# Optimization experiments

Hardware: AMD Instinct MI355X
Metric: run time of the kernel (lower is better)

The kernel has to match this reference:

```python
import jax, jax.numpy as jnp
import numpy as np

NUM_HEADS = 8
ATTN_DIM = 64

def setup_inputs() -> dict:
    key = jax.random.key(0)
    ks = jax.random.split(key, 16)
    C = ATTN_DIM
    inp = {
        "rgb_fea": jax.random.normal(ks[0], (2, C, 48, 48), jnp.float32),
        "depth_fea": jax.random.normal(ks[1], (2, 1, 24, 24), jnp.float32),
        # expend_conv: Conv2d(1 -> C, k=1), with bias (torch default)
        "w_exp": jax.random.normal(ks[2], (C, 1), jnp.float32) * 0.2,
        "b_exp": jax.random.normal(ks[3], (C,), jnp.float32) * 0.02,
        # q/k/v linears (no bias), weights stored torch-style [out, in]
        "w_rgb_q": jax.random.normal(ks[4], (C, C), jnp.float32) * (C ** -0.5),
        "w_rgb_k": jax.random.normal(ks[5], (C, C), jnp.float32) * (C ** -0.5),
        "w_rgb_v": jax.random.normal(ks[6], (C, C), jnp.float32) * (C ** -0.5),
        "w_dep_q": jax.random.normal(ks[7], (C, C), jnp.float32) * (C ** -0.5),
        "w_dep_k": jax.random.normal(ks[8], (C, C), jnp.float32) * (C ** -0.5),
        "w_dep_v": jax.random.normal(ks[9], (C, C), jnp.float32) * (C ** -0.5),
        # output projections (with bias)
        "w_rgb_proj": jax.random.normal(ks[10], (C, C), jnp.float32) * (C ** -0.5),
        "b_rgb_proj": jax.random.normal(ks[11], (C,), jnp.float32) * 0.02,
        "w_dep_proj": jax.random.normal(ks[12], (C, C), jnp.float32) * (C ** -0.5),
        "b_dep_proj": jax.random.normal(ks[13], (C,), jnp.float32) * 0.02,
        # compress_conv: Conv2d(2C -> C, k=1), with bias
        "w_comp": jax.random.normal(ks[14], (C, 2 * C), jnp.float32) * ((2 * C) ** -0.5),
        "b_comp": jax.random.normal(ks[15], (C,), jnp.float32) * 0.02,
    }
    return inp


def _heads(x, b, n, h):
    # [B, N, C] -> [B, H, N, C/H]
    c = x.shape[-1]
    return x.reshape(b, n, h, c // h).transpose(0, 2, 1, 3)


def reference(rgb_fea, depth_fea, w_exp, b_exp,
              w_rgb_q, w_rgb_k, w_rgb_v, w_dep_q, w_dep_k, w_dep_v,
              w_rgb_proj, b_rgb_proj, w_dep_proj, b_dep_proj,
              w_comp, b_comp):
    b, c, h, w = rgb_fea.shape
    H = NUM_HEADS
    scale = (c // H) ** -0.5

    # expend_conv (1x1) + ReLU + bilinear upsample (align_corners=False)
    d = jnp.einsum('bihw,oi->bohw', depth_fea, w_exp) + b_exp[None, :, None, None]
    d = jax.nn.relu(d)
    d = jax.image.resize(d, (b, c, h, w), method='bilinear')

    # (B,C,H,W) -> transpose(1,3) -> (B,W,H,C) -> (B, N=w*h, C)
    N = w * h
    rgb = rgb_fea.transpose(0, 3, 2, 1).reshape(b, N, c)
    dep = d.transpose(0, 3, 2, 1).reshape(b, N, c)

    rq = _heads(rgb @ w_rgb_q.T, b, N, H)
    rk = _heads(rgb @ w_rgb_k.T, b, N, H)
    rv = _heads(rgb @ w_rgb_v.T, b, N, H)
    dq = _heads(dep @ w_dep_q.T, b, N, H)
    dk = _heads(dep @ w_dep_k.T, b, N, H)
    dv = _heads(dep @ w_dep_v.T, b, N, H)

    # rgb queries attend to depth keys/values
    rgb_attn = jax.nn.softmax(jnp.einsum('bhnd,bhmd->bhnm', rq, dk) * scale, axis=-1)
    rgb_out = jnp.einsum('bhnm,bhmd->bhnd', rgb_attn, dv)
    rgb_out = rgb_out.transpose(0, 2, 1, 3).reshape(b, N, c) @ w_rgb_proj.T + b_rgb_proj

    # depth queries attend to rgb keys/values
    dep_attn = jax.nn.softmax(jnp.einsum('bhnd,bhmd->bhnm', dq, rk) * scale, axis=-1)
    dep_out = jnp.einsum('bhnm,bhmd->bhnd', dep_attn, rv)
    dep_out = dep_out.transpose(0, 2, 1, 3).reshape(b, N, c) @ w_dep_proj.T + b_dep_proj

    # (B,N,C) -> (B,C,N) -> (B,C,w,h)
    rgb_out = rgb_out.transpose(0, 2, 1).reshape(b, c, w, h)
    dep_out = dep_out.transpose(0, 2, 1).reshape(b, c, w, h)

    fuse = jnp.concatenate([rgb_out, dep_out], axis=1)
    fuse = jnp.einsum('bihw,oi->bohw', fuse, w_comp) + b_comp[None, :, None, None]
    return jax.nn.gelu(fuse, approximate=False)
```

## Files before the change

kernel.cpp:

```cpp
#include <hip/hip_runtime.h>
#include <math.h>

#define BATCH 2
#define C 64
#define HH 48
#define WW 48
#define NTOK 2304
#define HEADS 8
#define KVSTRIDE 12

typedef unsigned short bf16_t;
typedef __attribute__((ext_vector_type(8))) short bf16x8;
typedef __attribute__((ext_vector_type(4))) float f32x4;

__device__ __forceinline__ bf16_t f2bf(float f) {
    unsigned int u = __float_as_uint(f);
    u = (u + 0x7fffu + ((u >> 16) & 1u)) >> 16;
    return (bf16_t)u;
}
__device__ __forceinline__ unsigned pack2(float a, float b) {
    return (unsigned)f2bf(a) | ((unsigned)f2bf(b) << 16);
}
__device__ __forceinline__ float4 ld_bf4(const bf16_t* p) {
    uint2 v = *(const uint2*)p;
    float4 r;
    r.x = __uint_as_float(v.x << 16); r.y = __uint_as_float(v.x & 0xffff0000u);
    r.z = __uint_as_float(v.y << 16); r.w = __uint_as_float(v.y & 0xffff0000u);
    return r;
}

__device__ __forceinline__ void stage_x_row(
    float* xrow, const float* rgb, const float* dep,
    const float* w_exp, const float* b_exp,
    int b, int n, int strm, int c0, int cstep)
{
    int wi = n / HH, hi = n % HH;
    if (strm == 0) {
        const float* base = rgb + (size_t)b * C * NTOK + (size_t)hi * WW + wi;
        for (int c = c0; c < 64; c += cstep)
            xrow[c] = base[(size_t)c * NTOK];
    } else {
        float cy = 0.5f * hi - 0.25f, cx = 0.5f * wi - 0.25f;
        float fy0 = floorf(cy), fx0 = floorf(cx);
        float fy = cy - fy0, fx = cx - fx0;
        int y0 = max((int)fy0, 0), x0 = max((int)fx0, 0);
        int y1 = min((int)fy0 + 1, 23), x1 = min((int)fx0 + 1, 23);
        const float* dp = dep + b * 576;
        float d00 = dp[y0*24 + x0], d01 = dp[y0*24 + x1];
        float d10 = dp[y1*24 + x0], d11 = dp[y1*24 + x1];
        for (int c = c0; c < 64; c += cstep) {
            float w = w_exp[c], bb = b_exp[c];
            float r00 = fmaxf(w*d00 + bb, 0.f), r01 = fmaxf(w*d01 + bb, 0.f);
            float r10 = fmaxf(w*d10 + bb, 0.f), r11 = fmaxf(w*d11 + bb, 0.f);
            xrow[c] = (1.f-fy)*((1.f-fx)*r00 + fx*r01) + fy*((1.f-fx)*r10 + fx*r11);
        }
    }
}


__global__ __launch_bounds__(256) void wprep_kernel(
    const float* __restrict__ w_rp, const float* __restrict__ w_dp,
    const float* __restrict__ w_comp,
    const float* __restrict__ b_rp, const float* __restrict__ b_dp,
    const float* __restrict__ b_comp,
    float* __restrict__ W1, float* __restrict__ W2, float* __restrict__ beff)
{
    int bx = blockIdx.x, m = blockIdx.y;
    const float* Wp = m ? w_dp : w_rp;
    float* Wo = m ? W2 : W1;
    __shared__ float Wps[64][68];
    int tid = threadIdx.x;
    int sr = tid >> 4, sc4 = (tid & 15) * 4;
    #pragma unroll
    for (int rr = 0; rr < 4; ++rr) {
        int r = rr*16 + sr;
        *(float4*)&Wps[r][sc4] = *(const float4*)&Wp[r*64 + sc4];
    }
    __syncthreads();
    int r = tid >> 4;
    int o = bx*16 + r;
    int c4 = (tid & 15) * 4;
    float a0 = 0, a1 = 0, a2 = 0, a3 = 0;
    for (int j = 0; j < 64; ++j) {
        float wc = w_comp[o*128 + m*64 + j];
        float4 wp = *(const float4*)&Wps[j][c4];
        a0 += wc*wp.x; a1 += wc*wp.y; a2 += wc*wp.z; a3 += wc*wp.w;
    }
    Wo[o*64 + c4]     = a0;
    Wo[o*64 + c4 + 1] = a1;
    Wo[o*64 + c4 + 2] = a2;
    Wo[o*64 + c4 + 3] = a3;
    if (bx == 0 && m == 0 && tid < 64) {
        float s = b_comp[tid];
        for (int j = 0; j < 64; ++j)
            s += w_comp[tid*128 + j] * b_rp[j] + w_comp[tid*128 + 64 + j] * b_dp[j];
        beff[tid] = s;
    }
}

__global__ __launch_bounds__(256) void xprep_kernel(
    const float* __restrict__ rgb, const float* __restrict__ dep,
    const float* __restrict__ w_exp, const float* __restrict__ b_exp,
    float* __restrict__ Xt)
{
    int t = blockIdx.x;
    int z = blockIdx.y;
    int b = z >> 1, strm = z & 1;
    __shared__ float Ls[64][65];
    int tid = threadIdx.x;

    if (strm == 0) {
        const float* src = rgb + (size_t)b * C * NTOK + t * 64;
        #pragma unroll
        for (int p = 0; p < 4; ++p) {
            int idx = tid + p * 256;
            int c = idx >> 4, m4 = (idx & 15) * 4;
            *(float4*)&Ls[c][m4] = *(const float4*)&src[(size_t)c * NTOK + m4];
        }
        __syncthreads();
        #pragma unroll
        for (int p = 0; p < 4; ++p) {
            int idx = tid + p * 256;
            int row = idx >> 4, l = idx & 15;
            int mi = t * 64 + row;
            int hi = mi / 48, wi = mi % 48;
            int n  = wi * 48 + hi;
            float4 v;
            v.x = Ls[4*l + 0][row];
            v.y = Ls[4*l + 1][row];
            v.z = Ls[4*l + 2][row];
            v.w = Ls[4*l + 3][row];
            *(float4*)&Xt[((size_t)z * NTOK + n) * 64 + 4*l] = v;
        }
    } else {
        int tok_l = tid >> 2, cq = (tid & 3) * 16;
        int n = t * 64 + tok_l;
        int wi = n / HH, hi = n % HH;
        float cy = 0.5f * hi - 0.25f, cx = 0.5f * wi - 0.25f;
        float fy0 = floorf(cy), fx0 = floorf(cx);
        float fy = cy - fy0, fx = cx - fx0;
        int y0 = max((int)fy0, 0), x0 = max((int)fx0, 0);
        int y1 = min((int)fy0 + 1, 23), x1 = min((int)fx0 + 1, 23);
        const float* dp = dep + b * 576;
        float d00 = dp[y0*24 + x0], d01 = dp[y0*24 + x1];
        float d10 = dp[y1*24 + x0], d11 = dp[y1*24 + x1];
        float* orow = &Xt[((size_t)z * NTOK + n) * 64];
        #pragma unroll
        for (int cc = 0; cc < 16; cc += 4) {
            float4 v;
            #pragma unroll
            for (int j = 0; j < 4; ++j) {
                int c = cq + cc + j;
                float w = w_exp[c], bb = b_exp[c];
                float r00 = fmaxf(w*d00 + bb, 0.f), r01 = fmaxf(w*d01 + bb, 0.f);
                float r10 = fmaxf(w*d10 + bb, 0.f), r11 = fmaxf(w*d11 + bb, 0.f);
                float val = (1.f-fy)*((1.f-fx)*r00 + fx*r01) + fy*((1.f-fx)*r10 + fx*r11);
                ((float*)&v)[j] = val;
            }
            *(float4*)&orow[cq + cc] = v;
        }
    }
}

__global__ __launch_bounds__(256) void qkv_kernel(
    const float* __restrict__ Xt,
    const float* __restrict__ w_rq, const float* __restrict__ w_rk, const float* __restrict__ w_rv,
    const float* __restrict__ w_dq, const float* __restrict__ w_dk, const float* __restrict__ w_dv,
    bf16_t* __restrict__ Qb, bf16_t* __restrict__ Kb, bf16_t* __restrict__ VT)
{
    int tile = blockIdx.x;
    int z    = blockIdx.y;
    int b = z >> 1, strm = z & 1;
    int sb = strm*2 + b;

    __shared__ float Xs[32][68];
    __shared__ float Ws[64][68];
    int tid = threadIdx.x;
    #pragma unroll
    for (int p = 0; p < 2; ++p) {
        int idx = tid + p*256;
        int r = idx >> 4, c4 = (idx & 15) * 4;
        *(float4*)&Xs[r][c4] = *(const float4*)&Xt[((size_t)z*NTOK + tile*32 + r)*64 + c4];
    }
    int sr = tid >> 4, sc = (tid & 15) * 4;
    int ty = tid >> 4, tx = tid & 15;

    #pragma unroll
    for (int m = 0; m < 3; ++m) {
        const float* W = strm ? (m == 0 ? w_dq : m == 1 ? w_dk : w_dv)
                              : (m == 0 ? w_rq : m == 1 ? w_rk : w_rv);
        __syncthreads();
        #pragma unroll
        for (int rr = 0; rr < 4; ++rr) {
            int r = rr*16 + sr;
            *(float4*)&Ws[r][sc] = *(const float4*)&W[r*64 + sc];
        }
        __syncthreads();

        float acc[2][4] = {};
        #pragma unroll
        for (int k = 0; k < 64; k += 4) {
            float4 xv[2], wv4[4];
            #pragma unroll
            for (int i = 0; i < 2; ++i) xv[i] = *(const float4*)&Xs[2*ty + i][k];
            #pragma unroll
            for (int j = 0; j < 4; ++j) wv4[j] = *(const float4*)&Ws[tx + 16*j][k];
            #pragma unroll
            for (int i = 0; i < 2; ++i)
                #pragma unroll
                for (int j = 0; j < 4; ++j)
                    acc[i][j] += xv[i].x*wv4[j].x + xv[i].y*wv4[j].y + xv[i].z*wv4[j].z + xv[i].w*wv4[j].w;
        }
        float scale = (m == 0) ? (0.35355339059327373f * 1.4426950408889634f) : 1.0f;
        #pragma unroll
        for (int j = 0; j < 4; ++j) {
            int o = tx + 16*j;
            int h = o >> 3, d = o & 7;
            #pragma unroll
            for (int i = 0; i < 2; ++i) {
                int n = tile*32 + 2*ty + i;
                bf16_t v = f2bf(acc[i][j] * scale);
                if (m == 0)      Qb[(((size_t)sb*8 + h)*NTOK + n)*8 + d] = v;
                else if (m == 1) Kb[(((size_t)sb*8 + h)*NTOK + n)*8 + d] = v;
                else             VT[(((size_t)sb*8 + h)*8 + d)*NTOK + n] = v;
            }
        }
    }
}

__global__ __launch_bounds__(256) void attn_kernel(
    const bf16_t* __restrict__ Qb, const bf16_t* __restrict__ Kb,
    const bf16_t* __restrict__ VT,
    float* __restrict__ AOr, float* __restrict__ AOd)
{
    int h = blockIdx.y;
    int z = blockIdx.z;
    int b = z >> 1, which = z & 1;
    int qsb = which * 2 + b;
    int ksb = (1 - which) * 2 + b;
    const bf16_t* Q  = Qb + ((size_t)qsb * 8 + h) * NTOK * 8;
    const bf16_t* K  = Kb + ((size_t)ksb * 8 + h) * NTOK * 8;
    const bf16_t* Vt = VT + ((size_t)ksb * 8 + h) * 8 * NTOK;
    float* AO = which ? AOd : AOr;

    __shared__ __align__(16) bf16_t Pls[4][16][40];
    __shared__ __align__(16) float  Ols[4][16][16];

    int tid = threadIdx.x;
    int t = tid & 63, w = tid >> 6;
    int m16 = t & 15, quad = t >> 4;
    int qt = blockIdx.x * 4 + w;
    int n0 = qt * 16;

    const bf16x8 zf = {0,0,0,0,0,0,0,0};
    const bf16x8 onesf = {0x3F80,0x3F80,0x3F80,0x3F80,0x3F80,0x3F80,0x3F80,0x3F80};
    const f32x4 cz = {0.f, 0.f, 0.f, 0.f};

    bf16x8 qf = (quad == 0) ? *(const bf16x8*)&Q[(size_t)(n0 + m16) * 8] : zf;

    f32x4 oacc = cz;

    #pragma unroll 1
    for (int ck = 0; ck < 72; ++ck) {
        int k0 = ck * 32;
        bf16x8 kf0 = (quad == 0) ? *(const bf16x8*)&K[(size_t)(k0 + m16) * 8]      : zf;
        bf16x8 kf1 = (quad == 0) ? *(const bf16x8*)&K[(size_t)(k0 + 16 + m16) * 8] : zf;
        bf16x8 vf = (m16 < 8) ? *(const bf16x8*)&Vt[(size_t)m16 * NTOK + k0 + quad * 8]
                  : (m16 == 8 ? onesf : zf);

        f32x4 s0 = __builtin_amdgcn_mfma_f32_16x16x32_bf16(qf, kf0, cz, 0, 0, 0);
        f32x4 s1 = __builtin_amdgcn_mfma_f32_16x16x32_bf16(qf, kf1, cz, 0, 0, 0);

        #pragma unroll
        for (int r = 0; r < 4; ++r) {
            float p0 = __builtin_amdgcn_exp2f(s0[r]);
            float p1 = __builtin_amdgcn_exp2f(s1[r]);
            Pls[w][quad*4 + r][m16]      = (bf16_t)(__float_as_uint(p0) >> 16);
            Pls[w][quad*4 + r][m16 + 16] = (bf16_t)(__float_as_uint(p1) >> 16);
        }
        bf16x8 pf = *(const bf16x8*)&Pls[w][m16][quad * 8];
        oacc = __builtin_amdgcn_mfma_f32_16x16x32_bf16(pf, vf, oacc, 0, 0, 0);
    }

    #pragma unroll
    for (int r = 0; r < 4; ++r)
        Ols[w][quad*4 + r][m16] = oacc[r];
    #pragma unroll
    for (int e = 0; e < 2; ++e) {
        int idx = t * 2 + e;
        int qq = idx >> 3, d = idx & 7;
        float val = Ols[w][qq][d] / Ols[w][qq][8];
        AO[((size_t)b * NTOK + n0 + qq) * 64 + 8 * h + d] = val;
    }
}

__global__ __launch_bounds__(256) void outcomp_kernel(
    const float* __restrict__ AOr, const float* __restrict__ AOd,
    const float* __restrict__ W1, const float* __restrict__ W2,
    const float* __restrict__ beff, float* __restrict__ out)
{
    int tile = blockIdx.x;
    int b    = blockIdx.y;
    int n0 = tile * 32;
    __shared__ float Ar[32][68];
    __shared__ float Ad[32][68];
    __shared__ float W1s[64][68];
    __shared__ float W2s[64][68];
    int tid = threadIdx.x;
    #pragma unroll
    for (int pass = 0; pass < 2; ++pass) {
        int idx = tid + pass*256;
        int row = idx >> 4, c4 = (idx & 15) * 4;
        *(float4*)&Ar[row][c4] = *(const float4*)&AOr[((size_t)b*NTOK + n0 + row)*64 + c4];
        *(float4*)&Ad[row][c4] = *(const float4*)&AOd[((size_t)b*NTOK + n0 + row)*64 + c4];
    }
    {
        int sr = tid >> 4, sc4 = (tid & 15) * 4;
        #pragma unroll
        for (int rr = 0; rr < 4; ++rr) {
            int r = rr*16 + sr;
            *(float4*)&W1s[r][sc4] = *(const float4*)&W1[r*64 + sc4];
            *(float4*)&W2s[r][sc4] = *(const float4*)&W2[r*64 + sc4];
        }
    }
    __syncthreads();

    int tx = tid & 15, ty = tid >> 4;
    float g[2][4] = {};
    #pragma unroll
    for (int k = 0; k < 64; k += 4) {
        float4 xr0 = *(const float4*)&Ar[2*ty][k];
        float4 xr1 = *(const float4*)&Ar[2*ty + 1][k];
        float4 xd0 = *(const float4*)&Ad[2*ty][k];
        float4 xd1 = *(const float4*)&Ad[2*ty + 1][k];
        #pragma unroll
        for (int jj = 0; jj < 4; ++jj) {
            float4 w1 = *(const float4*)&W1s[tx + 16*jj][k];
            float4 w2 = *(const float4*)&W2s[tx + 16*jj][k];
            g[0][jj] += xr0.x*w1.x + xr0.y*w1.y + xr0.z*w1.z + xr0.w*w1.w
                      + xd0.x*w2.x + xd0.y*w2.y + xd0.z*w2.z + xd0.w*w2.w;
            g[1][jj] += xr1.x*w1.x + xr1.y*w1.y + xr1.z*w1.z + xr1.w*w1.w
                      + xd1.x*w2.x + xd1.y*w2.y + xd1.z*w2.z + xd1.w*w2.w;
        }
    }

    __syncthreads();
    float* Gs = &W1s[0][0];
    #pragma unroll
    for (int jj = 0; jj < 4; ++jj) {
        int o = tx + 16*jj;
        float be = beff[o];
        #pragma unroll
        for (int i = 0; i < 2; ++i) {
            float x = g[i][jj] + be;
            float gl = 0.5f * x * (1.0f + erff(x * 0.70710678118654752f));
            Gs[o*40 + 2*ty + i] = gl;
        }
    }
    __syncthreads();
    #pragma unroll
    for (int p = 0; p < 2; ++p) {
        int idx = tid + p*256;
        int o = idx >> 3, s = idx & 7;
        float4 v = *(const float4*)&Gs[o*40 + 4*s];
        *(float4*)&out[((size_t)(b*C + o))*NTOK + n0 + 4*s] = v;
    }
}

__global__ __launch_bounds__(256) void kv_all_kernel(
    const float* __restrict__ rgb, const float* __restrict__ dep,
    const float* __restrict__ w_exp, const float* __restrict__ b_exp,
    const float* __restrict__ w_rk, const float* __restrict__ w_rv,
    const float* __restrict__ w_dk, const float* __restrict__ w_dv,
    bf16_t* __restrict__ Kr, bf16_t* __restrict__ Vr,
    bf16_t* __restrict__ Kd, bf16_t* __restrict__ Vd)
{
    int tile = blockIdx.x;
    int m    = blockIdx.y;
    int z    = blockIdx.z;
    int b = z >> 1, strm = z & 1;
    const float* W = strm ? (m ? w_dv : w_dk) : (m ? w_rv : w_rk);
    bf16_t* O = (strm ? (m ? Vd : Kd) : (m ? Vr : Kr))
              + ((size_t)b * NTOK + tile * 64) * 64;

    __shared__ float Xs[64][68];
    __shared__ float Ws[64][68];
    int tid = threadIdx.x;
    {
        int r = tid & 63, c0 = tid >> 6;
        stage_x_row(&Xs[r][0], rgb, dep, w_exp, b_exp, b, tile*64 + r, strm, c0, 4);
    }
    int sr = tid >> 4, sc = (tid & 15) * 4;
    #pragma unroll
    for (int rr = 0; rr < 4; ++rr) {
        int r = rr*16 + sr;
        *(float4*)&Ws[r][sc] = *(const float4*)&W[r*64 + sc];
    }
    __syncthreads();

    int ty = tid >> 4, tx = tid & 15;
    float acc[4][4] = {};
    #pragma unroll
    for (int k = 0; k < 64; k += 4) {
        float4 xv[4], wv4[4];
        #pragma unroll
        for (int i = 0; i < 4; ++i) xv[i] = *(const float4*)&Xs[4*ty + i][k];
        #pragma unroll
        for (int j = 0; j < 4; ++j) wv4[j] = *(const float4*)&Ws[tx + 16*j][k];
        #pragma unroll
        for (int i = 0; i < 4; ++i)
            #pragma unroll
            for (int j = 0; j < 4; ++j)
                acc[i][j] += xv[i].x*wv4[j].x + xv[i].y*wv4[j].y + xv[i].z*wv4[j].z + xv[i].w*wv4[j].w;
    }
    #pragma unroll
    for (int i = 0; i < 4; ++i)
        #pragma unroll
        for (int j = 0; j < 4; ++j)
            O[(4*ty + i)*64 + tx + 16*j] = f2bf(acc[i][j]);
}

__global__ __launch_bounds__(256) void attn_all_kernel(
    const float* __restrict__ rgb, const float* __restrict__ dep,
    const float* __restrict__ w_exp, const float* __restrict__ b_exp,
    const float* __restrict__ w_rq, const float* __restrict__ w_dq,
    const bf16_t* __restrict__ Kr, const bf16_t* __restrict__ Vr,
    const bf16_t* __restrict__ Kd, const bf16_t* __restrict__ Vd,
    bf16_t* __restrict__ AOr, bf16_t* __restrict__ AOd)
{
    int qt = blockIdx.x;
    int h  = blockIdx.y;
    int z  = blockIdx.z;
    int b = z >> 1, which = z & 1;
    const float* wq = which ? w_dq : w_rq;
    const bf16_t* K = which ? Kr : Kd;
    const bf16_t* V = which ? Vr : Vd;
    bf16_t* AO      = which ? AOd : AOr;

    __shared__ float Xs[64][68];
    __shared__ float Wqs[8][64];
    __shared__ __align__(16) float Ks[4][64][KVSTRIDE];
    __shared__ __align__(16) float Vs[4][64][KVSTRIDE];

    int tid = threadIdx.x;
    int t = tid & 63;
    int w = tid >> 6;
    int n = qt * 64 + t;

    stage_x_row(&Xs[t][0], rgb, dep, w_exp, b_exp, b, n, which == 0 ? 0 : 1, w, 4);
    if (w == 0) {
        #pragma unroll
        for (int d = 0; d < 8; ++d) Wqs[d][t] = wq[(8*h + d)*64 + t];
    }
    __syncthreads();

    const float sc = 0.35355339059327373f * 1.4426950408889634f;
    float q[8];
    #pragma unroll
    for (int d = 0; d < 8; ++d) {
        float s = 0.f;
        #pragma unroll 8
        for (int c = 0; c < 64; ++c) s += Xs[t][c] * Wqs[d][c];
        q[d] = s * sc;
    }

    float mrun = -INFINITY, l = 0.f;
    float acc[8] = {};

    #pragma unroll 1
    for (int st = 0; st < 9; ++st) {
        __syncthreads();
        {
            size_t g = ((size_t)b * NTOK + (w*576 + st*64 + t)) * 64 + 8 * h;
            *(float4*)&Ks[w][t][0] = ld_bf4(&K[g]);
            *(float4*)&Ks[w][t][4] = ld_bf4(&K[g + 4]);
            *(float4*)&Vs[w][t][0] = ld_bf4(&V[g]);
            *(float4*)&Vs[w][t][4] = ld_bf4(&V[g + 4]);
        }
        __syncthreads();

        for (int g8 = 0; g8 < 8; ++g8) {
            float s[8];
            #pragma unroll
            for (int u = 0; u < 8; ++u) {
                const float4 ka = *(const float4*)&Ks[w][g8*8 + u][0];
                const float4 kb = *(const float4*)&Ks[w][g8*8 + u][4];
                s[u] = q[0]*ka.x + q[1]*ka.y + q[2]*ka.z + q[3]*ka.w
                     + q[4]*kb.x + q[5]*kb.y + q[6]*kb.z + q[7]*kb.w;
            }
            float tm = fmaxf(fmaxf(fmaxf(s[0],s[1]), fmaxf(s[2],s[3])),
                             fmaxf(fmaxf(s[4],s[5]), fmaxf(s[6],s[7])));
            float mn = fmaxf(mrun, tm);
            float alpha = __builtin_amdgcn_exp2f(mrun - mn);
            float ps = 0.f;
            #pragma unroll
            for (int u = 0; u < 8; ++u) { s[u] = __builtin_amdgcn_exp2f(s[u] - mn); ps += s[u]; }
            l = l * alpha + ps;
            #pragma unroll
            for (int d = 0; d < 8; ++d) acc[d] *= alpha;
            #pragma unroll
            for (int u = 0; u < 8; ++u) {
                const float4 va = *(const float4*)&Vs[w][g8*8 + u][0];
                const float4 vb = *(const float4*)&Vs[w][g8*8 + u][4];
                acc[0] += s[u]*va.x; acc[1] += s[u]*va.y; acc[2] += s[u]*va.z; acc[3] += s[u]*va.w;
                acc[4] += s[u]*vb.x; acc[5] += s[u]*vb.y; acc[6] += s[u]*vb.z; acc[7] += s[u]*vb.w;
            }
            mrun = mn;
        }
    }

    float* part = &Xs[0][0];
    __syncthreads();
    {
        float* p = &part[(w*64 + t) * 10];
        p[0] = mrun; p[1] = l;
        #pragma unroll
        for (int d = 0; d < 8; ++d) p[2 + d] = acc[d];
    }
    __syncthreads();
    if (tid < 64) {
        float M = -INFINITY;
        #pragma unroll
        for (int v = 0; v < 4; ++v) M = fmaxf(M, part[(v*64 + t)*10]);
        float L = 0.f, o[8] = {};
        #pragma unroll
        for (int v = 0; v < 4; ++v) {
            const float* p = &part[(v*64 + t)*10];
            float al = __builtin_amdgcn_exp2f(p[0] - M);
            L += p[1] * al;
            #pragma unroll
            for (int d = 0; d < 8; ++d) o[d] += p[2 + d] * al;
        }
        float inv = 1.0f / L;
        uint4 ov;
        ov.x = pack2(o[0]*inv, o[1]*inv);
        ov.y = pack2(o[2]*inv, o[3]*inv);
        ov.z = pack2(o[4]*inv, o[5]*inv);
        ov.w = pack2(o[6]*inv, o[7]*inv);
        *(uint4*)&AO[((size_t)b * NTOK + n) * 64 + 8 * h] = ov;
    }
}

__global__ __launch_bounds__(256) void projcomp_all_kernel(
    const bf16_t* __restrict__ AOr, const bf16_t* __restrict__ AOd,
    const float* __restrict__ w_rp, const float* __restrict__ b_rp,
    const float* __restrict__ w_dp, const float* __restrict__ b_dp,
    const float* __restrict__ w_comp, const float* __restrict__ b_comp,
    float* __restrict__ out)
{
    int tile = blockIdx.x;
    int b    = blockIdx.y;
    __shared__ float A[64][68];
    __shared__ float Bf[64][68];
    __shared__ float Pf[64][68];
    int tid = threadIdx.x;
    int sr = tid >> 4, sc = (tid & 15) * 4;
    int ty = tid >> 4, tx = tid & 15;
    float G[4][4] = {};

    #pragma unroll
    for (int half = 0; half < 2; ++half) {
        const bf16_t* AOx = half ? AOd : AOr;
        const float* Wp   = half ? w_dp : w_rp;
        const float* bp   = half ? b_dp : b_rp;
        #pragma unroll
        for (int rr = 0; rr < 4; ++rr) {
            int r = rr*16 + sr;
            *(float4*)&A[r][sc]  = ld_bf4(&AOx[((size_t)b*NTOK + tile*64 + r)*64 + sc]);
            *(float4*)&Bf[r][sc] = *(const float4*)&Wp[r*64 + sc];
        }
        __syncthreads();
        float acc[4][4] = {};
        #pragma unroll
        for (int k = 0; k < 64; k += 4) {
            float4 xv[4], wv[4];
            #pragma unroll
            for (int i = 0; i < 4; ++i) xv[i] = *(const float4*)&A[4*ty + i][k];
            #pragma unroll
            for (int j = 0; j < 4; ++j) wv[j] = *(const float4*)&Bf[tx + 16*j][k];
            #pragma unroll
            for (int i = 0; i < 4; ++i)
                #pragma unroll
                for (int j = 0; j < 4; ++j)
                    acc[i][j] += xv[i].x*wv[j].x + xv[i].y*wv[j].y + xv[i].z*wv[j].z + xv[i].w*wv[j].w;
        }
        __syncthreads();
        #pragma unroll
        for (int j = 0; j < 4; ++j) {
            float bj = bp[tx + 16*j];
            #pragma unroll
            for (int i = 0; i < 4; ++i)
                Pf[4*ty + i][tx + 16*j] = acc[i][j] + bj;
        }
        #pragma unroll
        for (int rr = 0; rr < 4; ++rr) {
            int r = rr*16 + sr;
            *(float4*)&Bf[r][sc] = *(const float4*)&w_comp[r*128 + half*64 + sc];
        }
        __syncthreads();
        #pragma unroll
        for (int k = 0; k < 64; k += 4) {
            float4 xv[4], wv[4];
            #pragma unroll
            for (int i = 0; i < 4; ++i) xv[i] = *(const float4*)&Pf[4*ty + i][k];
            #pragma unroll
            for (int j = 0; j < 4; ++j) wv[j] = *(const float4*)&Bf[tx + 16*j][k];
            #pragma unroll
            for (int i = 0; i < 4; ++i)
                #pragma unroll
                for (int j = 0; j < 4; ++j)
                    G[i][j] += xv[i].x*wv[j].x + xv[i].y*wv[j].y + xv[i].z*wv[j].z + xv[i].w*wv[j].w;
        }
        __syncthreads();
    }

    #pragma unroll
    for (int j = 0; j < 4; ++j) {
        int o = tx + 16*j;
        float bj = b_comp[o];
        #pragma unroll
        for (int i = 0; i < 4; ++i) {
            int n = tile*64 + 4*ty + i;
            int wi = n / HH, hi = n % HH;
            float x = G[i][j] + bj;
            float g = 0.5f * x * (1.0f + erff(x * 0.70710678118654752f));
            out[((b*C + o)*WW + wi)*HH + hi] = g;
        }
    }
}

extern "C" void kernel_launch(void* const* d_in, const int* in_sizes, int n_in,
                              void* d_out, int out_size, void* d_ws, size_t ws_size,
                              hipStream_t stream) {
    const float* rgb_fea = (const float*)d_in[0];
    const float* depth   = (const float*)d_in[1];
    const float* w_exp   = (const float*)d_in[2];
    const float* b_exp   = (const float*)d_in[3];
    const float* w_rq    = (const float*)d_in[4];
    const float* w_rk    = (const float*)d_in[5];
    const float* w_rv    = (const float*)d_in[6];
    const float* w_dq    = (const float*)d_in[7];
    const float* w_dk    = (const float*)d_in[8];
    const float* w_dv    = (const float*)d_in[9];
    const float* w_rp    = (const float*)d_in[10];
    const float* b_rp    = (const float*)d_in[11];
    const float* w_dp    = (const float*)d_in[12];
    const float* b_dp    = (const float*)d_in[13];
    const float* w_comp  = (const float*)d_in[14];
    const float* b_comp  = (const float*)d_in[15];
    float* out = (float*)d_out;

    if (ws_size >= 5931264) {
        char* Wb = (char*)d_ws;
        bf16_t* Qb  = (bf16_t*)Wb;
        bf16_t* Kb  = (bf16_t*)(Wb + 1179648);
        bf16_t* VT  = (bf16_t*)(Wb + 2359296);
        float* AOr  = (float*)(Wb + 3538944);
        float* AOd  = (float*)(Wb + 4718592);
        float* W1   = (float*)(Wb + 5898240);
        float* W2   = (float*)(Wb + 5914624);
        float* beff = (float*)(Wb + 5931008);
        float* Xt   = (float*)(Wb + 3538944);

        wprep_kernel<<<dim3(4, 2), dim3(256), 0, stream>>>(
            w_rp, w_dp, w_comp, b_rp, b_dp, b_comp, W1, W2, beff);
        xprep_kernel<<<dim3(36, 4), dim3(256), 0, stream>>>(
            rgb_fea, depth, w_exp, b_exp, Xt);
        qkv_kernel<<<dim3(72, 4), dim3(256), 0, stream>>>(
            Xt, w_rq, w_rk, w_rv, w_dq, w_dk, w_dv, Qb, Kb, VT);
        attn_kernel<<<dim3(36, 8, 4), dim3(256), 0, stream>>>(
            Qb, Kb, VT, AOr, AOd);
        outcomp_kernel<<<dim3(72, 2), dim3(256), 0, stream>>>(
            AOr, AOd, W1, W2, beff, out);
    } else {
        const size_t BUF = (size_t)BATCH * NTOK * 64;
        bf16_t* Kr  = (bf16_t*)d_ws;
        bf16_t* Vr  = Kr + BUF;
        bf16_t* Kd  = Vr + BUF;
        bf16_t* Vd  = Kd + BUF;
        bf16_t* AOr = Vd + BUF;
        bf16_t* AOd = AOr + BUF;
        kv_all_kernel<<<dim3(36, 2, 4), dim3(256), 0, stream>>>(
            rgb_fea, depth, w_exp, b_exp, w_rk, w_rv, w_dk, w_dv, Kr, Vr, Kd, Vd);
        attn_all_kernel<<<dim3(36, 8, 4), dim3(256), 0, stream>>>(
            rgb_fea, depth, w_exp, b_exp, w_rq, w_dq, Kr, Vr, Kd, Vd, AOr, AOd);
        projcomp_all_kernel<<<dim3(36, 2), dim3(256), 0, stream>>>(
            AOr, AOd, w_rp, b_rp, w_dp, b_dp, w_comp, b_comp, out);
    }
}
```

Measured before the change: 190.7 us.

## Split attention over key halves with atomic accumulation, merge prep kernels, widen grids

Attention now splits the key range into two halves per query tile. Each half accumulates unnormalized outputs and softmax denominators into zeroed buffers with atomicAdd, and the output kernel divides by the denominator. The weight-prep and input-prep kernels are merged into one launch, qkv gets a grid dimension per projection, and outcomp uses smaller tiles so more blocks run. The aim is to fill more compute units and cut launch overhead, at the cost of a memset, atomic traffic and an extra normalization pass. The split path is taken only if the workspace is at least 6226176 bytes.

```diff
diff --git a/kernel.cpp b/kernel.cpp
--- a/kernel.cpp
+++ b/kernel.cpp
@@ -58,111 +58,109 @@
 }
 
 
-__global__ __launch_bounds__(256) void wprep_kernel(
+__global__ __launch_bounds__(256) void prep_kernel(
+    const float* __restrict__ rgb, const float* __restrict__ dep,
+    const float* __restrict__ w_exp, const float* __restrict__ b_exp,
     const float* __restrict__ w_rp, const float* __restrict__ w_dp,
     const float* __restrict__ w_comp,
     const float* __restrict__ b_rp, const float* __restrict__ b_dp,
     const float* __restrict__ b_comp,
+    float* __restrict__ Xt,
     float* __restrict__ W1, float* __restrict__ W2, float* __restrict__ beff)
 {
-    int bx = blockIdx.x, m = blockIdx.y;
-    const float* Wp = m ? w_dp : w_rp;
-    float* Wo = m ? W2 : W1;
-    __shared__ float Wps[64][68];
+    __shared__ float U[64*68];
+    int bid = blockIdx.x;
     int tid = threadIdx.x;
-    int sr = tid >> 4, sc4 = (tid & 15) * 4;
-    #pragma unroll
-    for (int rr = 0; rr < 4; ++rr) {
-        int r = rr*16 + sr;
-        *(float4*)&Wps[r][sc4] = *(const float4*)&Wp[r*64 + sc4];
-    }
-    __syncthreads();
-    int r = tid >> 4;
-    int o = bx*16 + r;
-    int c4 = (tid & 15) * 4;
-    float a0 = 0, a1 = 0, a2 = 0, a3 = 0;
-    for (int j = 0; j < 64; ++j) {
-        float wc = w_comp[o*128 + m*64 + j];
-        float4 wp = *(const float4*)&Wps[j][c4];
-        a0 += wc*wp.x; a1 += wc*wp.y; a2 += wc*wp.z; a3 += wc*wp.w;
-    }
-    Wo[o*64 + c4]     = a0;
-    Wo[o*64 + c4 + 1] = a1;
-    Wo[o*64 + c4 + 2] = a2;
-    Wo[o*64 + c4 + 3] = a3;
-    if (bx == 0 && m == 0 && tid < 64) {
-        float s = b_comp[tid];
-        for (int j = 0; j < 64; ++j)
-            s += w_comp[tid*128 + j] * b_rp[j] + w_comp[tid*128 + 64 + j] * b_dp[j];
-        beff[tid] = s;
-    }
-}
-
-__global__ __launch_bounds__(256) void xprep_kernel(
-    const float* __restrict__ rgb, const float* __restrict__ dep,
-    const float* __restrict__ w_exp, const float* __restrict__ b_exp,
-    float* __restrict__ Xt)
-{
-    int t = blockIdx.x;
-    int z = blockIdx.y;
-    int b = z >> 1, strm = z & 1;
-    __shared__ float Ls[64][65];
-    int tid = threadIdx.x;
-
-    if (strm == 0) {
-        const float* src = rgb + (size_t)b * C * NTOK + t * 64;
-        #pragma unroll
-        for (int p = 0; p < 4; ++p) {
-            int idx = tid + p * 256;
-            int c = idx >> 4, m4 = (idx & 15) * 4;
-            *(float4*)&Ls[c][m4] = *(const float4*)&src[(size_t)c * NTOK + m4];
+
+    if (bid < 144) {
+        int t = bid >> 2, z = bid & 3;
+        int b = z >> 1, strm = z & 1;
+        if (strm == 0) {
+            const float* src = rgb + (size_t)b * C * NTOK + t * 64;
+            #pragma unroll
+            for (int p = 0; p < 4; ++p) {
+                int idx = tid + p * 256;
+                int c = idx >> 4, m4 = (idx & 15) * 4;
+                *(float4*)&U[c*65 + m4] = *(const float4*)&src[(size_t)c * NTOK + m4];
+            }
+            __syncthreads();
+            #pragma unroll
+            for (int p = 0; p < 4; ++p) {
+                int idx = tid + p * 256;
+                int row = idx >> 4, l = idx & 15;
+                int mi = t * 64 + row;
+                int hi = mi / 48, wi = mi % 48;
+                int n  = wi * 48 + hi;
+                float4 v;
+                v.x = U[(4*l + 0)*65 + row];
+                v.y = U[(4*l + 1)*65 + row];
+                v.z = U[(4*l + 2)*65 + row];
+                v.w = U[(4*l + 3)*65 + row];
+                *(float4*)&Xt[((size_t)z * NTOK + n) * 64 + 4*l] = v;
+            }
+        } else {
+            int tok_l = tid >> 2, cq = (tid & 3) * 16;
+            int n = t * 64 + tok_l;
+            int wi = n / HH, hi = n % HH;
+            float cy = 0.5f * hi - 0.25f, cx = 0.5f * wi - 0.25f;
+            float fy0 = floorf(cy), fx0 = floorf(cx);
+            float fy = cy - fy0, fx = cx - fx0;
+            int y0 = max((int)fy0, 0), x0 = max((int)fx0, 0);
+            int y1 = min((int)fy0 + 1, 23), x1 = min((int)fx0 + 1, 23);
+            const float* dp = dep + b * 576;
+            float d00 = dp[y0*24 + x0], d01 = dp[y0*24 + x1];
+            float d10 = dp[y1*24 + x0], d11 = dp[y1*24 + x1];
+            float* orow = &Xt[((size_t)z * NTOK + n) * 64];
+            #pragma unroll
+            for (int cc = 0; cc < 16; cc += 4) {
+                float4 v;
+                #pragma unroll
+                for (int j = 0; j < 4; ++j) {
+                    int c = cq + cc + j;
+                    float w = w_exp[c], bb = b_exp[c];
+                    float r00 = fmaxf(w*d00 + bb, 0.f), r01 = fmaxf(w*d01 + bb, 0.f);
+                    float r10 = fmaxf(w*d10 + bb, 0.f), r11 = fmaxf(w*d11 + bb, 0.f);
+                    float val = (1.f-fy)*((1.f-fx)*r00 + fx*r01) + fy*((1.f-fx)*r10 + fx*r11);
+                    ((float*)&v)[j] = val;
+                }
+                *(float4*)&orow[cq + cc] = v;
+            }
+        }
+    } else {
+        int idx0 = bid - 144;
+        int bx = idx0 & 3, m = idx0 >> 2;
+        const float* Wp = m ? w_dp : w_rp;
+        float* Wo = m ? W2 : W1;
+        int sr = tid >> 4, sc4 = (tid & 15) * 4;
+        #pragma unroll
+        for (int rr = 0; rr < 4; ++rr) {
+            int r = rr*16 + sr;
+            *(float4*)&U[r*68 + sc4] = *(const float4*)&Wp[r*64 + sc4];
         }
         __syncthreads();
-        #pragma unroll
-        for (int p = 0; p < 4; ++p) {
-            int idx = tid + p * 256;
-            int row = idx >> 4, l = idx & 15;
-            int mi = t * 64 + row;
-            int hi = mi / 48, wi = mi % 48;
-            int n  = wi * 48 + hi;
-            float4 v;
-            v.x = Ls[4*l + 0][row];
-            v.y = Ls[4*l + 1][row];
-            v.z = Ls[4*l + 2][row];
-            v.w = Ls[4*l + 3][row];
-            *(float4*)&Xt[((size_t)z * NTOK + n) * 64 + 4*l] = v;
-        }
-    } else {
-        int tok_l = tid >> 2, cq = (tid & 3) * 16;
-        int n = t * 64 + tok_l;
-        int wi = n / HH, hi = n % HH;
-        float cy = 0.5f * hi - 0.25f, cx = 0.5f * wi - 0.25f;
-        float fy0 = floorf(cy), fx0 = floorf(cx);
-        float fy = cy - fy0, fx = cx - fx0;
-        int y0 = max((int)fy0, 0), x0 = max((int)fx0, 0);
-        int y1 = min((int)fy0 + 1, 23), x1 = min((int)fx0 + 1, 23);
-        const float* dp = dep + b * 576;
-        float d00 = dp[y0*24 + x0], d01 = dp[y0*24 + x1];
-        float d10 = dp[y1*24 + x0], d11 = dp[y1*24 + x1];
-        float* orow = &Xt[((size_t)z * NTOK + n) * 64];
-        #pragma unroll
-        for (int cc = 0; cc < 16; cc += 4) {
-            float4 v;
-            #pragma unroll
-            for (int j = 0; j < 4; ++j) {
-                int c = cq + cc + j;
-                float w = w_exp[c], bb = b_exp[c];
-                float r00 = fmaxf(w*d00 + bb, 0.f), r01 = fmaxf(w*d01 + bb, 0.f);
-                float r10 = fmaxf(w*d10 + bb, 0.f), r11 = fmaxf(w*d11 + bb, 0.f);
-                float val = (1.f-fy)*((1.f-fx)*r00 + fx*r01) + fy*((1.f-fx)*r10 + fx*r11);
-                ((float*)&v)[j] = val;
-            }
-            *(float4*)&orow[cq + cc] = v;
-        }
-    }
-}
-
-__global__ __launch_bounds__(256) void qkv_kernel(
+        int r = tid >> 4;
+        int o = bx*16 + r;
+        int c4 = (tid & 15) * 4;
+        float a0 = 0, a1 = 0, a2 = 0, a3 = 0;
+        for (int j = 0; j < 64; ++j) {
+            float wc = w_comp[o*128 + m*64 + j];
+            float4 wp = *(const float4*)&U[j*68 + c4];
+            a0 += wc*wp.x; a1 += wc*wp.y; a2 += wc*wp.z; a3 += wc*wp.w;
+        }
+        Wo[o*64 + c4]     = a0;
+        Wo[o*64 + c4 + 1] = a1;
+        Wo[o*64 + c4 + 2] = a2;
+        Wo[o*64 + c4 + 3] = a3;
+        if (bx == 0 && m == 0 && tid < 64) {
+            float s = b_comp[tid];
+            for (int j = 0; j < 64; ++j)
+                s += w_comp[tid*128 + j] * b_rp[j] + w_comp[tid*128 + 64 + j] * b_dp[j];
+            beff[tid] = s;
+        }
+    }
+}
+
+__global__ __launch_bounds__(256, 2) void qkv_kernel(
     const float* __restrict__ Xt,
     const float* __restrict__ w_rq, const float* __restrict__ w_rk, const float* __restrict__ w_rv,
     const float* __restrict__ w_dq, const float* __restrict__ w_dk, const float* __restrict__ w_dv,
@@ -170,8 +168,11 @@
 {
     int tile = blockIdx.x;
     int z    = blockIdx.y;
+    int m    = blockIdx.z;
     int b = z >> 1, strm = z & 1;
     int sb = strm*2 + b;
+    const float* W = strm ? (m == 0 ? w_dq : m == 1 ? w_dk : w_dv)
+                          : (m == 0 ? w_rq : m == 1 ? w_rk : w_rv);
 
     __shared__ float Xs[32][68];
     __shared__ float Ws[64][68];
@@ -182,56 +183,52 @@
         int r = idx >> 4, c4 = (idx & 15) * 4;
         *(float4*)&Xs[r][c4] = *(const float4*)&Xt[((size_t)z*NTOK + tile*32 + r)*64 + c4];
     }
-    int sr = tid >> 4, sc = (tid & 15) * 4;
-    int ty = tid >> 4, tx = tid & 15;
-
-    #pragma unroll
-    for (int m = 0; m < 3; ++m) {
-        const float* W = strm ? (m == 0 ? w_dq : m == 1 ? w_dk : w_dv)
-                              : (m == 0 ? w_rq : m == 1 ? w_rk : w_rv);
-        __syncthreads();
+    {
+        int sr = tid >> 4, sc = (tid & 15) * 4;
         #pragma unroll
         for (int rr = 0; rr < 4; ++rr) {
             int r = rr*16 + sr;
             *(float4*)&Ws[r][sc] = *(const float4*)&W[r*64 + sc];
         }
-        __syncthreads();
-
-        float acc[2][4] = {};
-        #pragma unroll
-        for (int k = 0; k < 64; k += 4) {
-            float4 xv[2], wv4[4];
-            #pragma unroll
-            for (int i = 0; i < 2; ++i) xv[i] = *(const float4*)&Xs[2*ty + i][k];
-            #pragma unroll
-            for (int j = 0; j < 4; ++j) wv4[j] = *(const float4*)&Ws[tx + 16*j][k];
-            #pragma unroll
-            for (int i = 0; i < 2; ++i)
-                #pragma unroll
-                for (int j = 0; j < 4; ++j)
-                    acc[i][j] += xv[i].x*wv4[j].x + xv[i].y*wv4[j].y + xv[i].z*wv4[j].z + xv[i].w*wv4[j].w;
-        }
-        float scale = (m == 0) ? (0.35355339059327373f * 1.4426950408889634f) : 1.0f;
-        #pragma unroll
-        for (int j = 0; j < 4; ++j) {
-            int o = tx + 16*j;
-            int h = o >> 3, d = o & 7;
-            #pragma unroll
-            for (int i = 0; i < 2; ++i) {
-                int n = tile*32 + 2*ty + i;
-                bf16_t v = f2bf(acc[i][j] * scale);
-                if (m == 0)      Qb[(((size_t)sb*8 + h)*NTOK + n)*8 + d] = v;
-                else if (m == 1) Kb[(((size_t)sb*8 + h)*NTOK + n)*8 + d] = v;
-                else             VT[(((size_t)sb*8 + h)*8 + d)*NTOK + n] = v;
-            }
-        }
-    }
-}
-
-__global__ __launch_bounds__(256) void attn_kernel(
+    }
+    __syncthreads();
+
+    int ty = tid >> 4, tx = tid & 15;
+    float acc[2][4] = {};
+    #pragma unroll
+    for (int k = 0; k < 64; k += 4) {
+        float4 xv[2], wv4[4];
+        #pragma unroll
+        for (int i = 0; i < 2; ++i) xv[i] = *(const float4*)&Xs[2*ty + i][k];
+        #pragma unroll
+        for (int j = 0; j < 4; ++j) wv4[j] = *(const float4*)&Ws[tx + 16*j][k];
+        #pragma unroll
+        for (int i = 0; i < 2; ++i)
+            #pragma unroll
+            for (int j = 0; j < 4; ++j)
+                acc[i][j] += xv[i].x*wv4[j].x + xv[i].y*wv4[j].y + xv[i].z*wv4[j].z + xv[i].w*wv4[j].w;
+    }
+    float scale = (m == 0) ? (0.35355339059327373f * 1.4426950408889634f) : 1.0f;
+    #pragma unroll
+    for (int j = 0; j < 4; ++j) {
+        int o = tx + 16*j;
+        int h = o >> 3, d = o & 7;
+        #pragma unroll
+        for (int i = 0; i < 2; ++i) {
+            int n = tile*32 + 2*ty + i;
+            bf16_t v = f2bf(acc[i][j] * scale);
+            if (m == 0)      Qb[(((size_t)sb*8 + h)*NTOK + n)*8 + d] = v;
+            else if (m == 1) Kb[(((size_t)sb*8 + h)*NTOK + n)*8 + d] = v;
+            else             VT[(((size_t)sb*8 + h)*8 + d)*NTOK + n] = v;
+        }
+    }
+}
+
+__global__ __launch_bounds__(256) void attn_split_kernel(
     const bf16_t* __restrict__ Qb, const bf16_t* __restrict__ Kb,
     const bf16_t* __restrict__ VT,
-    float* __restrict__ AOr, float* __restrict__ AOd)
+    float* __restrict__ AOr, float* __restrict__ AOd,
+    float* __restrict__ Lr, float* __restrict__ Ld)
 {
     int h = blockIdx.y;
     int z = blockIdx.z;
@@ -242,6 +239,75 @@
     const bf16_t* K  = Kb + ((size_t)ksb * 8 + h) * NTOK * 8;
     const bf16_t* Vt = VT + ((size_t)ksb * 8 + h) * 8 * NTOK;
     float* AO = which ? AOd : AOr;
+    float* Lx = which ? Ld : Lr;
+
+    __shared__ __align__(16) bf16_t Pls[4][16][40];
+    __shared__ __align__(16) float  Ols[4][16][16];
+
+    int tid = threadIdx.x;
+    int t = tid & 63, w = tid >> 6;
+    int m16 = t & 15, quad = t >> 4;
+    int qt = (blockIdx.x >> 1) * 4 + w;
+    int kh = blockIdx.x & 1;
+    int n0 = qt * 16;
+
+    const bf16x8 zf = {0,0,0,0,0,0,0,0};
+    const bf16x8 onesf = {0x3F80,0x3F80,0x3F80,0x3F80,0x3F80,0x3F80,0x3F80,0x3F80};
+    const f32x4 cz = {0.f, 0.f, 0.f, 0.f};
+
+    bf16x8 qf = (quad == 0) ? *(const bf16x8*)&Q[(size_t)(n0 + m16) * 8] : zf;
+
+    f32x4 oacc = cz;
+
+    #pragma unroll 1
+    for (int ck = kh*36; ck < kh*36 + 36; ++ck) {
+        int k0 = ck * 32;
+        bf16x8 kf0 = (quad == 0) ? *(const bf16x8*)&K[(size_t)(k0 + m16) * 8]      : zf;
+        bf16x8 kf1 = (quad == 0) ? *(const bf16x8*)&K[(size_t)(k0 + 16 + m16) * 8] : zf;
+        bf16x8 vf = (m16 < 8) ? *(const bf16x8*)&Vt[(size_t)m16 * NTOK + k0 + quad * 8]
+                  : (m16 == 8 ? onesf : zf);
+
+        f32x4 s0 = __builtin_amdgcn_mfma_f32_16x16x32_bf16(qf, kf0, cz, 0, 0, 0);
+        f32x4 s1 = __builtin_amdgcn_mfma_f32_16x16x32_bf16(qf, kf1, cz, 0, 0, 0);
+
+        #pragma unroll
+        for (int r = 0; r < 4; ++r) {
+            float p0 = __builtin_amdgcn_exp2f(s0[r]);
+            float p1 = __builtin_amdgcn_exp2f(s1[r]);
+            Pls[w][quad*4 + r][m16]      = (bf16_t)(__float_as_uint(p0) >> 16);
+            Pls[w][quad*4 + r][m16 + 16] = (bf16_t)(__float_as_uint(p1) >> 16);
+        }
+        bf16x8 pf = *(const bf16x8*)&Pls[w][m16][quad * 8];
+        oacc = __builtin_amdgcn_mfma_f32_16x16x32_bf16(pf, vf, oacc, 0, 0, 0);
+    }
+
+    #pragma unroll
+    for (int r = 0; r < 4; ++r)
+        Ols[w][quad*4 + r][m16] = oacc[r];
+    #pragma unroll
+    for (int e = 0; e < 2; ++e) {
+        int idx = t * 2 + e;
+        int qq = idx >> 3, d = idx & 7;
+        atomicAdd(&AO[((size_t)b * NTOK + n0 + qq) * 64 + 8 * h + d], Ols[w][qq][d]);
+    }
+    if (t < 16)
+        atomicAdd(&Lx[((size_t)b * NTOK + n0 + t) * 8 + h], Ols[w][t][8]);
+}
+
+__global__ __launch_bounds__(256) void attn_kernel_t1(
+    const bf16_t* __restrict__ Qb, const bf16_t* __restrict__ Kb,
+    const bf16_t* __restrict__ VT,
+    float* __restrict__ AOr, float* __restrict__ AOd)
+{
+    int h = blockIdx.y;
+    int z = blockIdx.z;
+    int b = z >> 1, which = z & 1;
+    int qsb = which * 2 + b;
+    int ksb = (1 - which) * 2 + b;
+    const bf16_t* Q  = Qb + ((size_t)qsb * 8 + h) * NTOK * 8;
+    const bf16_t* K  = Kb + ((size_t)ksb * 8 + h) * NTOK * 8;
+    const bf16_t* Vt = VT + ((size_t)ksb * 8 + h) * 8 * NTOK;
+    float* AO = which ? AOd : AOr;
 
     __shared__ __align__(16) bf16_t Pls[4][16][40];
     __shared__ __align__(16) float  Ols[4][16][16];
@@ -257,7 +323,6 @@
     const f32x4 cz = {0.f, 0.f, 0.f, 0.f};
 
     bf16x8 qf = (quad == 0) ? *(const bf16x8*)&Q[(size_t)(n0 + m16) * 8] : zf;
-
     f32x4 oacc = cz;
 
     #pragma unroll 1
@@ -294,25 +359,33 @@
     }
 }
 
-__global__ __launch_bounds__(256) void outcomp_kernel(
+__global__ __launch_bounds__(256, 2) void outcomp_kernel(
     const float* __restrict__ AOr, const float* __restrict__ AOd,
+    const float* __restrict__ Lr, const float* __restrict__ Ld,
     const float* __restrict__ W1, const float* __restrict__ W2,
     const float* __restrict__ beff, float* __restrict__ out)
 {
     int tile = blockIdx.x;
     int b    = blockIdx.y;
-    int n0 = tile * 32;
-    __shared__ float Ar[32][68];
-    __shared__ float Ad[32][68];
+    int n0 = tile * 16;
+    __shared__ float Ar[16][68];
+    __shared__ float Ad[16][68];
     __shared__ float W1s[64][68];
     __shared__ float W2s[64][68];
     int tid = threadIdx.x;
-    #pragma unroll
-    for (int pass = 0; pass < 2; ++pass) {
-        int idx = tid + pass*256;
-        int row = idx >> 4, c4 = (idx & 15) * 4;
-        *(float4*)&Ar[row][c4] = *(const float4*)&AOr[((size_t)b*NTOK + n0 + row)*64 + c4];
-        *(float4*)&Ad[row][c4] = *(const float4*)&AOd[((size_t)b*NTOK + n0 + row)*64 + c4];
+    {
+        int row = tid >> 4, c4 = (tid & 15) * 4;
+        size_t base = (size_t)b*NTOK + n0 + row;
+        float4 vr = *(const float4*)&AOr[base*64 + c4];
+        float4 vd = *(const float4*)&AOd[base*64 + c4];
+        if (Lr) {
+            float ir = 1.0f / Lr[base*8 + (c4 >> 3)];
+            float id = 1.0f / Ld[base*8 + (c4 >> 3)];
+            vr.x *= ir; vr.y *= ir; vr.z *= ir; vr.w *= ir;
+            vd.x *= id; vd.y *= id; vd.z *= id; vd.w *= id;
+        }
+        *(float4*)&Ar[row][c4] = vr;
+        *(float4*)&Ad[row][c4] = vd;
     }
     {
         int sr = tid >> 4, sc4 = (tid & 15) * 4;
@@ -326,21 +399,17 @@
     __syncthreads();
 
     int tx = tid & 15, ty = tid >> 4;
-    float g[2][4] = {};
+    float g[4] = {};
     #pragma unroll
     for (int k = 0; k < 64; k += 4) {
-        float4 xr0 = *(const float4*)&Ar[2*ty][k];
-        float4 xr1 = *(const float4*)&Ar[2*ty + 1][k];
-        float4 xd0 = *(const float4*)&Ad[2*ty][k];
-        float4 xd1 = *(const float4*)&Ad[2*ty + 1][k];
+        float4 xr = *(const float4*)&Ar[ty][k];
+        float4 xd = *(const float4*)&Ad[ty][k];
         #pragma unroll
         for (int jj = 0; jj < 4; ++jj) {
             float4 w1 = *(const float4*)&W1s[tx + 16*jj][k];
             float4 w2 = *(const float4*)&W2s[tx + 16*jj][k];
-            g[0][jj] += xr0.x*w1.x + xr0.y*w1.y + xr0.z*w1.z + xr0.w*w1.w
-                      + xd0.x*w2.x + xd0.y*w2.y + xd0.z*w2.z + xd0.w*w2.w;
-            g[1][jj] += xr1.x*w1.x + xr1.y*w1.y + xr1.z*w1.z + xr1.w*w1.w
-                      + xd1.x*w2.x + xd1.y*w2.y + xd1.z*w2.z + xd1.w*w2.w;
+            g[jj] += xr.x*w1.x + xr.y*w1.y + xr.z*w1.z + xr.w*w1.w
+                   + xd.x*w2.x + xd.y*w2.y + xd.z*w2.z + xd.w*w2.w;
         }
     }
 
@@ -349,20 +418,14 @@
     #pragma unroll
     for (int jj = 0; jj < 4; ++jj) {
         int o = tx + 16*jj;
-        float be = beff[o];
-        #pragma unroll
-        for (int i = 0; i < 2; ++i) {
-            float x = g[i][jj] + be;
-            float gl = 0.5f * x * (1.0f + erff(x * 0.70710678118654752f));
-            Gs[o*40 + 2*ty + i] = gl;
-        }
+        float x = g[jj] + beff[o];
+        float gl = 0.5f * x * (1.0f + erff(x * 0.70710678118654752f));
+        Gs[o*20 + ty] = gl;
     }
     __syncthreads();
-    #pragma unroll
-    for (int p = 0; p < 2; ++p) {
-        int idx = tid + p*256;
-        int o = idx >> 3, s = idx & 7;
-        float4 v = *(const float4*)&Gs[o*40 + 4*s];
+    {
+        int o = tid >> 2, s = tid & 3;
+        float4 v = *(const float4*)&Gs[o*20 + 4*s];
         *(float4*)&out[((size_t)(b*C + o))*NTOK + n0 + 4*s] = v;
     }
 }
@@ -650,7 +713,31 @@
     const float* b_comp  = (const float*)d_in[15];
     float* out = (float*)d_out;
 
-    if (ws_size >= 5931264) {
+    if (ws_size >= 6226176) {
+        char* Wb = (char*)d_ws;
+        bf16_t* Qb  = (bf16_t*)Wb;
+        bf16_t* Kb  = (bf16_t*)(Wb + 1179648);
+        bf16_t* VT  = (bf16_t*)(Wb + 2359296);
+        float* AOr  = (float*)(Wb + 3538944);
+        float* AOd  = (float*)(Wb + 4718592);
+        float* Lr   = (float*)(Wb + 5898240);
+        float* Ld   = (float*)(Wb + 6045696);
+        float* W1   = (float*)(Wb + 6193152);
+        float* W2   = (float*)(Wb + 6209536);
+        float* beff = (float*)(Wb + 6225920);
+        float* Xt   = (float*)(Wb + 3538944);
+
+        prep_kernel<<<dim3(152), dim3(256), 0, stream>>>(
+            rgb_fea, depth, w_exp, b_exp, w_rp, w_dp, w_comp,
+            b_rp, b_dp, b_comp, Xt, W1, W2, beff);
+        qkv_kernel<<<dim3(72, 4, 3), dim3(256), 0, stream>>>(
+            Xt, w_rq, w_rk, w_rv, w_dq, w_dk, w_dv, Qb, Kb, VT);
+        hipMemsetAsync(Wb + 3538944, 0, 2654208, stream);
+        attn_split_kernel<<<dim3(72, 8, 4), dim3(256), 0, stream>>>(
+            Qb, Kb, VT, AOr, AOd, Lr, Ld);
+        outcomp_kernel<<<dim3(144, 2), dim3(256), 0, stream>>>(
+            AOr, AOd, Lr, Ld, W1, W2, beff, out);
+    } else if (ws_size >= 5931264) {
         char* Wb = (char*)d_ws;
         bf16_t* Qb  = (bf16_t*)Wb;
         bf16_t* Kb  = (bf16_t*)(Wb + 1179648);
@@ -662,16 +749,16 @@
         float* beff = (float*)(Wb + 5931008);
         float* Xt   = (float*)(Wb + 3538944);
 
-        wprep_kernel<<<dim3(4, 2), dim3(256), 0, stream>>>(
-            w_rp, w_dp, w_comp, b_rp, b_dp, b_comp, W1, W2, beff);
-        xprep_kernel<<<dim3(36, 4), dim3(256), 0, stream>>>(
-            rgb_fea, depth, w_exp, b_exp, Xt);
-        qkv_kernel<<<dim3(72, 4), dim3(256), 0, stream>>>(
+        prep_kernel<<<dim3(152), dim3(256), 0, stream>>>(
+            rgb_fea, depth, w_exp, b_exp, w_rp, w_dp, w_comp,
+            b_rp, b_dp, b_comp, Xt, W1, W2, beff);
+        qkv_kernel<<<dim3(72, 4, 3), dim3(256), 0, stream>>>(
             Xt, w_rq, w_rk, w_rv, w_dq, w_dk, w_dv, Qb, Kb, VT);
-        attn_kernel<<<dim3(36, 8, 4), dim3(256), 0, stream>>>(
+        attn_kernel_t1<<<dim3(36, 8, 4), dim3(256), 0, stream>>>(
             Qb, Kb, VT, AOr, AOd);
-        outcomp_kernel<<<dim3(72, 2), dim3(256), 0, stream>>>(
-            AOr, AOd, W1, W2, beff, out);
+        outcomp_kernel<<<dim3(144, 2), dim3(256), 0, stream>>>(
+            AOr, AOd, (const float*)nullptr, (const float*)nullptr,
+            W1, W2, beff, out);
     } else {
         const size_t BUF = (size_t)BATCH * NTOK * 64;
         bf16_t* Kr  = (bf16_t*)d_ws;
```

After: 204.7 us. +7.3%, slower.
